# Optimization experiments

Hardware: AMD Instinct MI355X
Metric: run time of the kernel (lower is better)

The kernel has to match this reference:

```python
import jax, jax.numpy as jnp
import numpy as np
from jax import lax

K_SIZE = 5  # box filter window (odd)

def _box_sum(a, k):
    # Sum over a k x k window centered on each pixel, with edge clipping
    # (SAME padding => out-of-bounds contributes 0, matching the loop bounds).
    return lax.reduce_window(a, 0.0, lax.add,
                             window_dimensions=(1, 1, k, k),
                             window_strides=(1, 1, 1, 1),
                             padding='SAME')

def setup_inputs() -> dict:
    key = jax.random.key(0)
    x = jax.random.normal(key, (32, 3, 512, 512), dtype=jnp.float32)
    return {"x": x}

def reference(x) -> jnp.ndarray:
    # Edge-clipped mean filter: divide window sum by the number of valid
    # (in-bounds) pixels in each window, exactly as the original's `total`.
    sums = _box_sum(x, K_SIZE)
    counts = _box_sum(jnp.ones_like(x), K_SIZE)
    return sums / counts
```

## Files before the change

kernel.cpp:

```cpp
#include <hip/hip_runtime.h>

#define IMG   512
#define H     16
#define TPB   128
#define NXCD  8

__global__ __launch_bounds__(TPB)
void mean_filter_strip(const float* __restrict__ in, float* __restrict__ out,
                       int nstrips, int cpx) {
    __shared__ __align__(16) float vs[2][IMG + 8];

    const int hw  = blockIdx.x;
    const int bid = (hw % NXCD) * cpx + (hw / NXCD);
    const int plane = bid / nstrips;
    const int strip = bid - plane * nstrips;
    const int y0 = strip * H;
    const int x4 = threadIdx.x * 4;

    const float* __restrict__ src = in  + (size_t)plane * IMG * IMG + x4;
    float*       __restrict__ dst = out + (size_t)plane * IMG * IMG + x4;

    if (threadIdx.x < 2) {
        vs[threadIdx.x][2]   = 0.0f;
        vs[threadIdx.x][3]   = 0.0f;
        vs[threadIdx.x][516] = 0.0f;
        vs[threadIdx.x][517] = 0.0f;
    }

    float invcx[4];
    #pragma unroll
    for (int j = 0; j < 4; ++j) {
        const int x  = x4 + j;
        const int cx = min(x + 2, IMG - 1) - max(x - 2, 0) + 1;
        invcx[j] = 1.0f / (float)cx;
    }

    auto loadrow = [&](int y) -> float4 {
        if ((unsigned)y < (unsigned)IMG)
            return *(const float4*)(src + (size_t)y * IMG);
        return make_float4(0.0f, 0.0f, 0.0f, 0.0f);
    };

    float4 r0v, r1v, r2v, r3v, r4v;
    r1v = loadrow(y0 - 2);
    r2v = loadrow(y0 - 1);
    r3v = loadrow(y0);
    r4v = loadrow(y0 + 1);

    #pragma unroll
    for (int i = 0; i < H; ++i) {
        const int y = y0 + i;
        r0v = r1v; r1v = r2v; r2v = r3v; r3v = r4v;
        r4v = loadrow(y + 2);

        float4 v;
        v.x = r0v.x + r1v.x + r2v.x + r3v.x + r4v.x;
        v.y = r0v.y + r1v.y + r2v.y + r3v.y + r4v.y;
        v.z = r0v.z + r1v.z + r2v.z + r3v.z + r4v.z;
        v.w = r0v.w + r1v.w + r2v.w + r3v.w + r4v.w;

        const int b = i & 1;
        *(float4*)&vs[b][4 + x4] = v;
        __syncthreads();

        const float l0 = vs[b][x4 + 2];
        const float l1 = vs[b][x4 + 3];
        const float q0 = vs[b][x4 + 8];
        const float q1 = vs[b][x4 + 9];

        const int   cy    = min(y + 2, IMG - 1) - max(y - 2, 0) + 1;
        const float invcy = 1.0f / (float)cy;

        float4 o;
        o.x = (l0 + l1 + v.x + v.y + v.z) * (invcy * invcx[0]);
        o.y = (l1 + v.x + v.y + v.z + v.w) * (invcy * invcx[1]);
        o.z = (v.x + v.y + v.z + v.w + q0) * (invcy * invcx[2]);
        o.w = (v.y + v.z + v.w + q0 + q1) * (invcy * invcx[3]);

        *(float4*)(dst + (size_t)y * IMG) = o;
    }
}

extern "C" void kernel_launch(void* const* d_in, const int* in_sizes, int n_in,
                              void* d_out, int out_size, void* d_ws, size_t ws_size,
                              hipStream_t stream) {
    const float* x = (const float*)d_in[0];
    float* out = (float*)d_out;
    const int planes  = in_sizes[0] / (IMG * IMG);
    const int nstrips = IMG / H;
    const int nwg     = planes * nstrips;
    const int cpx     = nwg / NXCD;
    mean_filter_strip<<<dim3(nwg), dim3(TPB), 0, stream>>>(x, out, nstrips, cpx);
}
```

Baseline: 35.81 us.

## Use single-wave blocks with lane shuffles instead of LDS and barriers

```diff
diff --git a/kernel.cpp b/kernel.cpp
--- a/kernel.cpp
+++ b/kernel.cpp
@@ -1,83 +1,84 @@
 #include <hip/hip_runtime.h>
 
 #define IMG   512
-#define H     16
-#define TPB   128
+#define H     8
 #define NXCD  8
 
-__global__ __launch_bounds__(TPB)
-void mean_filter_strip(const float* __restrict__ in, float* __restrict__ out,
-                       int nstrips, int cpx) {
-    __shared__ __align__(16) float vs[2][IMG + 8];
-
+__global__ __launch_bounds__(64)
+void mean_filter_wave(const float* __restrict__ in, float* __restrict__ out,
+                      int nstrips, int cpx) {
     const int hw  = blockIdx.x;
     const int bid = (hw % NXCD) * cpx + (hw / NXCD);
     const int plane = bid / nstrips;
     const int strip = bid - plane * nstrips;
-    const int y0 = strip * H;
-    const int x4 = threadIdx.x * 4;
+    const int y0   = strip * H;
+    const int lane = threadIdx.x;
+    const int x8   = lane * 8;
 
-    const float* __restrict__ src = in  + (size_t)plane * IMG * IMG + x4;
-    float*       __restrict__ dst = out + (size_t)plane * IMG * IMG + x4;
+    const float* __restrict__ src = in  + (size_t)plane * IMG * IMG + x8;
+    float*       __restrict__ dst = out + (size_t)plane * IMG * IMG + x8;
 
-    if (threadIdx.x < 2) {
-        vs[threadIdx.x][2]   = 0.0f;
-        vs[threadIdx.x][3]   = 0.0f;
-        vs[threadIdx.x][516] = 0.0f;
-        vs[threadIdx.x][517] = 0.0f;
-    }
-
-    float invcx[4];
-    #pragma unroll
-    for (int j = 0; j < 4; ++j) {
-        const int x  = x4 + j;
+    float invcx[8];
+#pragma unroll
+    for (int j = 0; j < 8; ++j) {
+        const int x  = x8 + j;
         const int cx = min(x + 2, IMG - 1) - max(x - 2, 0) + 1;
         invcx[j] = 1.0f / (float)cx;
     }
 
-    auto loadrow = [&](int y) -> float4 {
-        if ((unsigned)y < (unsigned)IMG)
-            return *(const float4*)(src + (size_t)y * IMG);
-        return make_float4(0.0f, 0.0f, 0.0f, 0.0f);
+    float4 a0, a1, a2, a3, a4, b0, b1, b2, b3, b4;
+    auto loadrow = [&](int y, float4& a, float4& b) {
+        if ((unsigned)y < (unsigned)IMG) {
+            a = *(const float4*)(src + (size_t)y * IMG);
+            b = *(const float4*)(src + (size_t)y * IMG + 4);
+        } else {
+            a = make_float4(0.f, 0.f, 0.f, 0.f);
+            b = make_float4(0.f, 0.f, 0.f, 0.f);
+        }
     };
 
-    float4 r0v, r1v, r2v, r3v, r4v;
-    r1v = loadrow(y0 - 2);
-    r2v = loadrow(y0 - 1);
-    r3v = loadrow(y0);
-    r4v = loadrow(y0 + 1);
+    loadrow(y0 - 2, a1, b1);
+    loadrow(y0 - 1, a2, b2);
+    loadrow(y0,     a3, b3);
+    loadrow(y0 + 1, a4, b4);
 
-    #pragma unroll
+#pragma unroll
     for (int i = 0; i < H; ++i) {
         const int y = y0 + i;
-        r0v = r1v; r1v = r2v; r2v = r3v; r3v = r4v;
-        r4v = loadrow(y + 2);
+        a0 = a1; b0 = b1; a1 = a2; b1 = b2; a2 = a3; b2 = b3; a3 = a4; b3 = b4;
+        loadrow(y + 2, a4, b4);
 
-        float4 v;
-        v.x = r0v.x + r1v.x + r2v.x + r3v.x + r4v.x;
-        v.y = r0v.y + r1v.y + r2v.y + r3v.y + r4v.y;
-        v.z = r0v.z + r1v.z + r2v.z + r3v.z + r4v.z;
-        v.w = r0v.w + r1v.w + r2v.w + r3v.w + r4v.w;
+        const float v0 = a0.x + a1.x + a2.x + a3.x + a4.x;
+        const float v1 = a0.y + a1.y + a2.y + a3.y + a4.y;
+        const float v2 = a0.z + a1.z + a2.z + a3.z + a4.z;
+        const float v3 = a0.w + a1.w + a2.w + a3.w + a4.w;
+        const float v4 = b0.x + b1.x + b2.x + b3.x + b4.x;
+        const float v5 = b0.y + b1.y + b2.y + b3.y + b4.y;
+        const float v6 = b0.z + b1.z + b2.z + b3.z + b4.z;
+        const float v7 = b0.w + b1.w + b2.w + b3.w + b4.w;
 
-        const int b = i & 1;
-        *(float4*)&vs[b][4 + x4] = v;
-        __syncthreads();
-
-        const float l0 = vs[b][x4 + 2];
-        const float l1 = vs[b][x4 + 3];
-        const float q0 = vs[b][x4 + 8];
-        const float q1 = vs[b][x4 + 9];
+        float l0 = __shfl_up(v6, 1);
+        float l1 = __shfl_up(v7, 1);
+        float q0 = __shfl_down(v0, 1);
+        float q1 = __shfl_down(v1, 1);
+        if (lane == 0)  { l0 = 0.f; l1 = 0.f; }
+        if (lane == 63) { q0 = 0.f; q1 = 0.f; }
 
         const int   cy    = min(y + 2, IMG - 1) - max(y - 2, 0) + 1;
         const float invcy = 1.0f / (float)cy;
 
-        float4 o;
-        o.x = (l0 + l1 + v.x + v.y + v.z) * (invcy * invcx[0]);
-        o.y = (l1 + v.x + v.y + v.z + v.w) * (invcy * invcx[1]);
-        o.z = (v.x + v.y + v.z + v.w + q0) * (invcy * invcx[2]);
-        o.w = (v.y + v.z + v.w + q0 + q1) * (invcy * invcx[3]);
+        float4 oa, ob;
+        oa.x = (l0 + l1 + v0 + v1 + v2) * (invcy * invcx[0]);
+        oa.y = (l1 + v0 + v1 + v2 + v3) * (invcy * invcx[1]);
+        oa.z = (v0 + v1 + v2 + v3 + v4) * (invcy * invcx[2]);
+        oa.w = (v1 + v2 + v3 + v4 + v5) * (invcy * invcx[3]);
+        ob.x = (v2 + v3 + v4 + v5 + v6) * (invcy * invcx[4]);
+        ob.y = (v3 + v4 + v5 + v6 + v7) * (invcy * invcx[5]);
+        ob.z = (v4 + v5 + v6 + v7 + q0) * (invcy * invcx[6]);
+        ob.w = (v5 + v6 + v7 + q0 + q1) * (invcy * invcx[7]);
 
-        *(float4*)(dst + (size_t)y * IMG) = o;
+        *(float4*)(dst + (size_t)y * IMG)     = oa;
+        *(float4*)(dst + (size_t)y * IMG + 4) = ob;
     }
 }
 
@@ -90,5 +91,5 @@
     const int nstrips = IMG / H;
     const int nwg     = planes * nstrips;
     const int cpx     = nwg / NXCD;
-    mean_filter_strip<<<dim3(nwg), dim3(TPB), 0, stream>>>(x, out, nstrips, cpx);
+    mean_filter_wave<<<dim3(nwg), dim3(64), 0, stream>>>(x, out, nstrips, cpx);
 }
```

Result: slower. 42.81 us (+19.5%).
